# Optimization experiments

Hardware: AMD Instinct MI355X
Metric: run time of the kernel (lower is better)

The kernel has to match this reference:

```python
import jax, jax.numpy as jnp
import numpy as np

START_TAG = 8
STOP_TAG = 9
NEG_INF = -10000.0


def setup_inputs() -> dict:
    key = jax.random.key(0)
    k1, k2, k3 = jax.random.split(key, 3)
    S, B, T = 2048, 4096, 10
    feats = jax.random.normal(k1, (S, B, T), dtype=jnp.float32)
    lengths = jax.random.randint(k2, (B,), 1, S + 1, dtype=jnp.int32)
    transitions = jax.random.normal(k3, (T, T), dtype=jnp.float32)
    # transitions[next, prev]; nothing transitions INTO start, nothing OUT of stop
    transitions = transitions.at[START_TAG, :].set(NEG_INF).at[:, STOP_TAG].set(NEG_INF)
    return {"feats": feats, "transitions": transitions, "lengths": lengths}


def reference(feats, transitions, lengths):
    # Viterbi decode (the module's forward).
    S, B, T = feats.shape
    bidx = jnp.arange(B)
    init = jnp.full((B, T), NEG_INF, feats.dtype).at[:, START_TAG].set(0.0)

    def step(fv, feat):
        # fv: [B, T_prev]; transitions: [T_next, T_prev]
        ntv = fv[:, None, :] + transitions[None, :, :]      # [B, Tn, Tp]
        best = jnp.argmax(ntv, axis=2).astype(jnp.int32)    # [B, Tn]
        fv_new = jnp.max(ntv, axis=2) + feat                # [B, Tn]
        return fv_new, (fv_new, best)

    _, (fv_steps, bptrs) = jax.lax.scan(step, init, feats)
    fv_all = jnp.concatenate([init[None], fv_steps], axis=0)  # [S+1, B, T]

    last_fv = fv_all[lengths, bidx, :]                       # [B, T]
    terminal = last_fv + transitions[STOP_TAG][None, :]
    path_score = jnp.max(terminal, axis=1)                   # [B]
    best_last = jnp.argmax(terminal, axis=1).astype(jnp.int32)

    # Vectorized backtrace over all batches, scanning time in reverse.
    def bt_step(cur, j):
        nxt_j = jnp.minimum(j + 1, S - 1)
        gathered = bptrs[nxt_j, bidx, cur]                   # [B]
        cur_new = jnp.where(j == lengths - 1, best_last,
                  jnp.where(j < lengths - 1, gathered, cur))
        path_j = jnp.where(j < lengths, cur_new, 0)
        return cur_new, path_j

    _, paths_rev = jax.lax.scan(bt_step, best_last, jnp.arange(S - 1, -1, -1))
    best_paths = paths_rev[::-1].T                           # [B, S]
    return path_score, best_paths
```

## Files before the change

### kernel.cpp

```cpp
#include <hip/hip_runtime.h>
#include <stdint.h>
#include <stddef.h>

#define S_LEN 2048
#define B_N   4096
#define T_N   10
#define NCH   128
#define NEG_INF_F (-10000.0f)

template<int CTRL>
__device__ __forceinline__ int dppi(int v) {
    return __builtin_amdgcn_update_dpp(0, v, CTRL, 0xF, 0xF, true);
}

static __device__ __forceinline__ int imin(int a, int b) { return a < b ? a : b; }
static __device__ __forceinline__ int imax(int a, int b) { return a > b ? a : b; }

static __device__ __forceinline__ float vmax3(float a, float b, float c) {
    float d;
    asm("v_max3_f32 %0, %1, %2, %3" : "=v"(d) : "v"(a), "v"(b), "v"(c));
    return d;
}

__global__ void __launch_bounds__(256) viterbi_fwd(const float* __restrict__ feats,
                                                   const float* __restrict__ trans,
                                                   const int* __restrict__ lengths,
                                                   float* __restrict__ ckpt) {
    const float FNINF = __int_as_float(0xff800000);
    const int tid = threadIdx.x;
    const int t   = tid & 15;
    const int b   = blockIdx.x * 16 + (tid >> 4);
    const bool act = (t < T_N);
    const int len = lengths[b];

    int lenW = len;
    lenW = imax(lenW, __shfl_xor(lenW, 16, 64));
    lenW = imax(lenW, __shfl_xor(lenW, 32, 64));
    lenW = __builtin_amdgcn_readfirstlane(lenW);

    int q[16];
    q[0]  = t;
    q[1]  = dppi<0x121>(t);  q[2]  = dppi<0x122>(t);  q[3]  = dppi<0x123>(t);
    q[4]  = dppi<0x124>(t);  q[5]  = dppi<0x125>(t);  q[6]  = dppi<0x126>(t);
    q[7]  = dppi<0x127>(t);  q[8]  = dppi<0x128>(t);  q[9]  = dppi<0x129>(t);
    q[10] = dppi<0x12A>(t);  q[11] = dppi<0x12B>(t);  q[12] = dppi<0x12C>(t);
    q[13] = dppi<0x12D>(t);  q[14] = dppi<0x12E>(t);  q[15] = dppi<0x12F>(t);

    float trr[16];
    #pragma unroll
    for (int r = 0; r < 16; ++r) {
        bool v = act && (q[r] < T_N);
        trr[r] = v ? trans[t * T_N + q[r]] : FNINF;
    }

    const float* fptr = feats + (size_t)b * T_N + imin(t, T_N - 1);
    auto ldfeat = [&](int s) -> float {
        return fptr[(size_t)imin(s, S_LEN - 1) * (B_N * T_N)];
    };

    float fvr;
    {
        float finit = (t == 8) ? 0.0f : NEG_INF_F;
        asm("v_mov_b32 %0, %1\n\ts_nop 1" : "=v"(fvr) : "v"(finit));
    }

    float fA[8], fB[8];
    #pragma unroll
    for (int u = 0; u < 8; ++u) fA[u] = ldfeat(u);

    for (int s0 = 0; s0 < lenW; s0 += 8) {
        #pragma unroll
        for (int u = 0; u < 8; ++u) fB[u] = ldfeat(s0 + 8 + u);

        #pragma unroll
        for (int u = 0; u < 8; ++u) {
            float cd[16];
            cd[0] = fvr + trr[0];
#define DPPADD(N, S) asm("v_add_f32_dpp %0, %1, %2 " S " row_mask:0xf bank_mask:0xf" \
                         : "=v"(cd[N]) : "v"(fvr), "v"(trr[N]))
            DPPADD(1,  "row_ror:1");  DPPADD(2,  "row_ror:2");  DPPADD(3,  "row_ror:3");
            DPPADD(4,  "row_ror:4");  DPPADD(5,  "row_ror:5");  DPPADD(6,  "row_ror:6");
            DPPADD(7,  "row_ror:7");  DPPADD(8,  "row_ror:8");  DPPADD(9,  "row_ror:9");
            DPPADD(10, "row_ror:10"); DPPADD(11, "row_ror:11"); DPPADD(12, "row_ror:12");
            DPPADD(13, "row_ror:13"); DPPADD(14, "row_ror:14"); DPPADD(15, "row_ror:15");
#undef DPPADD
            float x0 = vmax3(cd[0],  cd[1],  cd[2]);
            float x1 = vmax3(cd[3],  cd[4],  cd[5]);
            float x2 = vmax3(cd[6],  cd[7],  cd[8]);
            float x3 = vmax3(cd[9],  cd[10], cd[11]);
            float x4 = vmax3(cd[12], cd[13], cd[14]);
            float y0 = vmax3(x0, x1, x2);
            float y1 = vmax3(x3, x4, cd[15]);
            float mm = fmaxf(y0, y1);
            asm("v_add_f32 %0, %1, %2\n\ts_nop 1" : "=v"(fvr) : "v"(mm), "v"(fA[u]));
        }

        const int snext = s0 + 8;
        if ((snext & 15) == 0) {
            if (act && snext <= len && snext <= S_LEN - 16)
                ckpt[((size_t)(snext >> 4) * B_N + b) * T_N + t] = fvr;
        }
        #pragma unroll
        for (int u = 0; u < 8; ++u) fA[u] = fB[u];
    }
}

__global__ void __launch_bounds__(256) bt_maps(const float* __restrict__ feats,
                                               const float* __restrict__ trans,
                                               const int* __restrict__ lengths,
                                               const float* __restrict__ ckpt,
                                               unsigned* __restrict__ bpd,
                                               unsigned char* __restrict__ bpb,
                                               uint2* __restrict__ gmap,
                                               float* __restrict__ lastfv) {
    const int c = blockIdx.x >> 4;
    const int b = ((blockIdx.x & 15) << 8) + threadIdx.x;
    const int len = lengths[b];
    const int r0 = c * 16;
    const int kl = len - r0;

    if (kl < 0) {
        gmap[(size_t)c * B_N + b] = make_uint2(0x76543210u, 0x98u);
        return;
    }

    float fv[T_N];
    if (c == 0) {
        #pragma unroll
        for (int p = 0; p < T_N; ++p) fv[p] = (p == 8) ? 0.0f : NEG_INF_F;
    } else {
        #pragma unroll
        for (int p = 0; p < T_N; ++p) fv[p] = ckpt[((size_t)c * B_N + b) * T_N + p];
    }

    float* lfp = lastfv + (size_t)b * T_N;
    if (kl == 0) {
        #pragma unroll
        for (int n = 0; n < T_N; ++n) lfp[n] = fv[n];
        gmap[(size_t)c * B_N + b] = make_uint2(0x76543210u, 0x98u);
        return;
    }

    const size_t rstride = (size_t)B_N * T_N;
    const float* fbase = feats + (size_t)b * T_N;

    float buf[T_N];
    {
        const float2* p2 = (const float2*)(fbase + (size_t)r0 * rstride);
        #pragma unroll
        for (int i = 0; i < 5; ++i) { float2 v = p2[i]; buf[2*i] = v.x; buf[2*i+1] = v.y; }
    }

    unsigned Glo = 0x76543210u, Ghi = 0x98u;

    {
        float m[T_N];
        #pragma unroll
        for (int n = 0; n < T_N; ++n) {
            float cd[T_N];
            #pragma unroll
            for (int p = 0; p < T_N; ++p) cd[p] = fv[p] + trans[n * T_N + p];
            float x0 = vmax3(cd[0], cd[1], cd[2]);
            float x1 = vmax3(cd[3], cd[4], cd[5]);
            float x2 = vmax3(cd[6], cd[7], cd[8]);
            m[n] = fmaxf(vmax3(x0, x1, x2), cd[9]);
        }
        #pragma unroll
        for (int n = 0; n < T_N; ++n) fv[n] = m[n] + buf[n];
    }

    #pragma unroll 1
    for (int k = 1; k <= 16; ++k) {
        const int r = r0 + k;
        {
            const float2* p2 = (const float2*)(fbase + (size_t)imin(r, S_LEN - 1) * rstride);
            #pragma unroll
            for (int i = 0; i < 5; ++i) { float2 v = p2[i]; buf[2*i] = v.x; buf[2*i+1] = v.y; }
        }
        if (k == kl) {
            #pragma unroll
            for (int n = 0; n < T_N; ++n) lfp[n] = fv[n];
        }
        unsigned mlo = 0, mhi = 0, nGlo = 0, nGhi = 0;
        unsigned long long G64 = ((unsigned long long)Ghi << 32) | Glo;
        float m[T_N];
        #pragma unroll
        for (int n = 0; n < T_N; ++n) {
            float cd[T_N];
            #pragma unroll
            for (int p = 0; p < T_N; ++p) cd[p] = fv[p] + trans[n * T_N + p];
            float x0 = vmax3(cd[0], cd[1], cd[2]);
            float x1 = vmax3(cd[3], cd[4], cd[5]);
            float x2 = vmax3(cd[6], cd[7], cd[8]);
            float mm = fmaxf(vmax3(x0, x1, x2), cd[9]);
            m[n] = mm;
            int ix = 9;
            #pragma unroll
            for (int p = 8; p >= 0; --p) ix = (cd[p] == mm) ? p : ix;
            unsigned nib = (unsigned)(G64 >> (ix << 2)) & 15u;
            if (n < 8) { mlo |= (unsigned)ix << (4 * n);       nGlo |= nib << (4 * n); }
            else       { mhi |= (unsigned)ix << (4 * (n - 8)); nGhi |= nib << (4 * (n - 8)); }
        }
        if (r < len) {
            bpd[(size_t)r * B_N + b] = mlo;
            bpb[(size_t)r * B_N + b] = (unsigned char)mhi;
            Glo = nGlo; Ghi = nGhi;
        }
        if (k < 16) {
            #pragma unroll
            for (int n = 0; n < T_N; ++n) fv[n] = m[n] + buf[n];
        }
    }

    gmap[(size_t)c * B_N + b] = make_uint2(Glo, Ghi);
}

static __device__ __forceinline__ int bpapply(uint2 w, int cur) {
    unsigned long long w64 = ((unsigned long long)w.y << 32) | (unsigned long long)w.x;
    return (int)((w64 >> (cur * 4)) & 15ULL);
}

__global__ void __launch_bounds__(256) bt_compose(const uint2* __restrict__ gmap,
                                                  const float* __restrict__ lastfv,
                                                  const float* __restrict__ trans,
                                                  unsigned char* __restrict__ entry,
                                                  float* __restrict__ score) {
    const int b = blockIdx.x * 256 + threadIdx.x;

    float term[T_N];
    #pragma unroll
    for (int n = 0; n < T_N; ++n)
        term[n] = lastfv[(size_t)b * T_N + n] + trans[9 * T_N + n];
    float x0 = vmax3(term[0], term[1], term[2]);
    float x1 = vmax3(term[3], term[4], term[5]);
    float x2 = vmax3(term[6], term[7], term[8]);
    float pm = fmaxf(vmax3(x0, x1, x2), term[9]);
    int st = 9;
    #pragma unroll
    for (int n = 8; n >= 0; --n) st = (term[n] == pm) ? n : st;
    score[b] = pm;

    uint2 wA[16], wB[16];
    auto pre = [&](uint2 (&W)[16], int cb) {
        #pragma unroll
        for (int u = 0; u < 16; ++u) W[u] = gmap[(size_t)(cb * 16 + u) * B_N + b];
    };
    auto proc = [&](uint2 (&W)[16], int cb) {
        #pragma unroll
        for (int u = 15; u >= 0; --u) {
            int cc = cb * 16 + u;
            entry[(size_t)cc * B_N + b] = (unsigned char)st;
            st = bpapply(W[u], st);
        }
    };
    pre(wA, 7);
    pre(wB, 6); proc(wA, 7);
    pre(wA, 5); proc(wB, 6);
    pre(wB, 4); proc(wA, 5);
    pre(wA, 3); proc(wB, 4);
    pre(wB, 2); proc(wA, 3);
    pre(wA, 1); proc(wB, 2);
    pre(wB, 0); proc(wA, 1);
    proc(wB, 0);
}

__global__ void __launch_bounds__(256) bt_emit(const unsigned* __restrict__ bpd,
                                               const unsigned char* __restrict__ bpb,
                                               const int* __restrict__ lengths,
                                               const unsigned char* __restrict__ entry,
                                               float* __restrict__ opaths) {
    const int c = blockIdx.x >> 4;
    const int b = ((blockIdx.x & 15) << 8) + threadIdx.x;
    const int len = lengths[b];
    float* op = opaths + (size_t)b * S_LEN + c * 16;

    if (c * 16 >= len) {
        float4 z = make_float4(0.f, 0.f, 0.f, 0.f);
        #pragma unroll
        for (int qq = 0; qq < 4; ++qq) *(float4*)(op + qq * 4) = z;
        return;
    }

    const int r0 = c * 16 + 1;
    unsigned Wd[16], Wb[16];
    #pragma unroll
    for (int u = 0; u < 16; ++u) {
        int r = r0 + u;
        unsigned d = 0x76543210u, h = 0x98u;
        if (r < len) { d = bpd[(size_t)r * B_N + b]; h = bpb[(size_t)r * B_N + b]; }
        Wd[u] = d; Wb[u] = h;
    }

    int cur = entry[(size_t)c * B_N + b];
    float buf[16];
    #pragma unroll
    for (int u = 15; u >= 0; --u) {
        unsigned long long w = ((unsigned long long)Wb[u] << 32) | Wd[u];
        cur = (int)((w >> ((cur * 4) & 63)) & 15ULL);
        buf[u] = (c * 16 + u < len) ? (float)cur : 0.0f;
    }
    #pragma unroll
    for (int qq = 0; qq < 4; ++qq)
        *(float4*)(op + qq * 4) = make_float4(buf[qq*4+0], buf[qq*4+1], buf[qq*4+2], buf[qq*4+3]);
}

extern "C" void kernel_launch(void* const* d_in, const int* in_sizes, int n_in,
                              void* d_out, int out_size, void* d_ws, size_t ws_size,
                              hipStream_t stream) {
    const float* feats   = (const float*)d_in[0];
    const float* trans   = (const float*)d_in[1];
    const int*   lengths = (const int*)d_in[2];
    float* out = (float*)d_out;

    char* w = (char*)d_ws;
    float*         ckpt  = (float*)w;          w += (size_t)NCH * B_N * T_N * 4;
    unsigned*      bpd   = (unsigned*)w;       w += (size_t)(S_LEN + 1) * B_N * 4;
    unsigned char* bpb   = (unsigned char*)w;  w += (size_t)(S_LEN + 1) * B_N;
    uint2*         gmap  = (uint2*)w;          w += (size_t)NCH * B_N * 8;
    unsigned char* entry = (unsigned char*)w;  w += (size_t)NCH * B_N;
    float*         lastfv = (float*)w;

    viterbi_fwd<<<B_N / 16, 256, 0, stream>>>(feats, trans, lengths, ckpt);
    bt_maps   <<<NCH * (B_N / 256), 256, 0, stream>>>(feats, trans, lengths, ckpt, bpd, bpb, gmap, lastfv);
    bt_compose<<<B_N / 256, 256, 0, stream>>>(gmap, lastfv, trans, entry, out);
    bt_emit   <<<NCH * (B_N / 256), 256, 0, stream>>>(bpd, bpb, lengths, entry, out + B_N);
}
```

Baseline: 338.3 us.

## Remap forward Viterbi to four lanes per batch with quad-permute DPP

The forward pass now gives each batch element a group of 4 lanes instead of 16. Tags 0-7 are spread across the quad as two per lane, and tags 8 and 9 are replicated in every lane. Each step uses quad_perm DPP shuffles and per-lane transition registers to compute the max over 10 predecessors for 4 output tags. This removes the 6 idle lanes out of every 16 and cuts the wave count by four (64-thread blocks). In exchange each lane does more arithmetic per step and holds larger feature prefetch buffers (32 floats each), which raises register pressure.

```diff
diff --git a/kernel.cpp b/kernel.cpp
--- a/kernel.cpp
+++ b/kernel.cpp
@@ -12,6 +12,10 @@
 __device__ __forceinline__ int dppi(int v) {
     return __builtin_amdgcn_update_dpp(0, v, CTRL, 0xF, 0xF, true);
 }
+template<int CTRL>
+__device__ __forceinline__ float dppf(float v) {
+    return __int_as_float(dppi<CTRL>(__float_as_int(v)));
+}
 
 static __device__ __forceinline__ int imin(int a, int b) { return a < b ? a : b; }
 static __device__ __forceinline__ int imax(int a, int b) { return a > b ? a : b; }
@@ -22,86 +26,100 @@
     return d;
 }
 
-__global__ void __launch_bounds__(256) viterbi_fwd(const float* __restrict__ feats,
-                                                   const float* __restrict__ trans,
-                                                   const int* __restrict__ lengths,
-                                                   float* __restrict__ ckpt) {
-    const float FNINF = __int_as_float(0xff800000);
+#define QP1 0x39
+#define QP2 0x4E
+#define QP3 0x93
+
+__global__ void __launch_bounds__(64) viterbi_fwd(const float* __restrict__ feats,
+                                                  const float* __restrict__ trans,
+                                                  const int* __restrict__ lengths,
+                                                  float* __restrict__ ckpt) {
     const int tid = threadIdx.x;
-    const int t   = tid & 15;
-    const int b   = blockIdx.x * 16 + (tid >> 4);
-    const bool act = (t < T_N);
+    const int l   = tid & 3;
+    const int b   = blockIdx.x * 16 + (tid >> 2);
     const int len = lengths[b];
 
     int lenW = len;
+    lenW = imax(lenW, __shfl_xor(lenW, 4, 64));
+    lenW = imax(lenW, __shfl_xor(lenW, 8, 64));
     lenW = imax(lenW, __shfl_xor(lenW, 16, 64));
     lenW = imax(lenW, __shfl_xor(lenW, 32, 64));
     lenW = __builtin_amdgcn_readfirstlane(lenW);
 
-    int q[16];
-    q[0]  = t;
-    q[1]  = dppi<0x121>(t);  q[2]  = dppi<0x122>(t);  q[3]  = dppi<0x123>(t);
-    q[4]  = dppi<0x124>(t);  q[5]  = dppi<0x125>(t);  q[6]  = dppi<0x126>(t);
-    q[7]  = dppi<0x127>(t);  q[8]  = dppi<0x128>(t);  q[9]  = dppi<0x129>(t);
-    q[10] = dppi<0x12A>(t);  q[11] = dppi<0x12B>(t);  q[12] = dppi<0x12C>(t);
-    q[13] = dppi<0x12D>(t);  q[14] = dppi<0x12E>(t);  q[15] = dppi<0x12F>(t);
-
-    float trr[16];
-    #pragma unroll
-    for (int r = 0; r < 16; ++r) {
-        bool v = act && (q[r] < T_N);
-        trr[r] = v ? trans[t * T_N + q[r]] : FNINF;
-    }
-
-    const float* fptr = feats + (size_t)b * T_N + imin(t, T_N - 1);
-    auto ldfeat = [&](int s) -> float {
-        return fptr[(size_t)imin(s, S_LEN - 1) * (B_N * T_N)];
-    };
-
-    float fvr;
-    {
-        float finit = (t == 8) ? 0.0f : NEG_INF_F;
-        asm("v_mov_b32 %0, %1\n\ts_nop 1" : "=v"(fvr) : "v"(finit));
-    }
-
-    float fA[8], fB[8];
-    #pragma unroll
-    for (int u = 0; u < 8; ++u) fA[u] = ldfeat(u);
-
-    for (int s0 = 0; s0 < lenW; s0 += 8) {
-        #pragma unroll
-        for (int u = 0; u < 8; ++u) fB[u] = ldfeat(s0 + 8 + u);
-
+    const int q1 = dppi<QP1>(l);
+    const int q2 = dppi<QP2>(l);
+    const int q3 = dppi<QP3>(l);
+
+    int to[4] = { l, 4 + l, 8, 9 };
+    float trAs[4], trA1[4], trA2[4], trA3[4];
+    float trBs[4], trB1[4], trB2[4], trB3[4];
+    float tr8[4], tr9[4];
+    #pragma unroll
+    for (int o = 0; o < 4; ++o) {
+        const float* tr = trans + to[o] * T_N;
+        trAs[o] = tr[l];      trA1[o] = tr[q1];     trA2[o] = tr[q2];     trA3[o] = tr[q3];
+        trBs[o] = tr[4 + l];  trB1[o] = tr[4 + q1]; trB2[o] = tr[4 + q2]; trB3[o] = tr[4 + q3];
+        tr8[o]  = tr[8];      tr9[o]  = tr[9];
+    }
+
+    float a = NEG_INF_F, bv = NEG_INF_F, f8 = 0.0f, f9 = NEG_INF_F;
+
+    const float* fp = feats + (size_t)b * T_N;
+    auto ldf = [&](int s, int k) -> float {
+        return fp[(size_t)imin(s, S_LEN - 1) * (B_N * T_N) + to[k]];
+    };
+
+    float fA[32], fB[32];
+    #pragma unroll
+    for (int u = 0; u < 8; ++u) {
+        #pragma unroll
+        for (int k = 0; k < 4; ++k) fA[u * 4 + k] = ldf(u, k);
+    }
+
+    auto onestep = [&](const float* f) {
+        float rA1 = dppf<QP1>(a),  rA2 = dppf<QP2>(a),  rA3 = dppf<QP3>(a);
+        float rB1 = dppf<QP1>(bv), rB2 = dppf<QP2>(bv), rB3 = dppf<QP3>(bv);
+        float m[4];
+        #pragma unroll
+        for (int o = 0; o < 4; ++o) {
+            float c0 = a   + trAs[o], c1 = rA1 + trA1[o], c2 = rA2 + trA2[o], c3 = rA3 + trA3[o];
+            float c4 = bv  + trBs[o], c5 = rB1 + trB1[o], c6 = rB2 + trB2[o], c7 = rB3 + trB3[o];
+            float c8 = f8 + tr8[o],   c9 = f9 + tr9[o];
+            float x0 = vmax3(c0, c1, c2);
+            float x1 = vmax3(c3, c4, c5);
+            float x2 = vmax3(c6, c7, c8);
+            m[o] = fmaxf(vmax3(x0, x1, x2), c9);
+        }
+        a  = m[0] + f[0];
+        bv = m[1] + f[1];
+        f8 = m[2] + f[2];
+        f9 = m[3] + f[3];
+    };
+    auto step8 = [&](float (&f)[32]) {
+        #pragma unroll
+        for (int u = 0; u < 8; ++u) onestep(&f[u * 4]);
+    };
+    auto loadinto = [&](float (&f)[32], int sbase) {
         #pragma unroll
         for (int u = 0; u < 8; ++u) {
-            float cd[16];
-            cd[0] = fvr + trr[0];
-#define DPPADD(N, S) asm("v_add_f32_dpp %0, %1, %2 " S " row_mask:0xf bank_mask:0xf" \
-                         : "=v"(cd[N]) : "v"(fvr), "v"(trr[N]))
-            DPPADD(1,  "row_ror:1");  DPPADD(2,  "row_ror:2");  DPPADD(3,  "row_ror:3");
-            DPPADD(4,  "row_ror:4");  DPPADD(5,  "row_ror:5");  DPPADD(6,  "row_ror:6");
-            DPPADD(7,  "row_ror:7");  DPPADD(8,  "row_ror:8");  DPPADD(9,  "row_ror:9");
-            DPPADD(10, "row_ror:10"); DPPADD(11, "row_ror:11"); DPPADD(12, "row_ror:12");
-            DPPADD(13, "row_ror:13"); DPPADD(14, "row_ror:14"); DPPADD(15, "row_ror:15");
-#undef DPPADD
-            float x0 = vmax3(cd[0],  cd[1],  cd[2]);
-            float x1 = vmax3(cd[3],  cd[4],  cd[5]);
-            float x2 = vmax3(cd[6],  cd[7],  cd[8]);
-            float x3 = vmax3(cd[9],  cd[10], cd[11]);
-            float x4 = vmax3(cd[12], cd[13], cd[14]);
-            float y0 = vmax3(x0, x1, x2);
-            float y1 = vmax3(x3, x4, cd[15]);
-            float mm = fmaxf(y0, y1);
-            asm("v_add_f32 %0, %1, %2\n\ts_nop 1" : "=v"(fvr) : "v"(mm), "v"(fA[u]));
-        }
-
-        const int snext = s0 + 8;
-        if ((snext & 15) == 0) {
-            if (act && snext <= len && snext <= S_LEN - 16)
-                ckpt[((size_t)(snext >> 4) * B_N + b) * T_N + t] = fvr;
-        }
-        #pragma unroll
-        for (int u = 0; u < 8; ++u) fA[u] = fB[u];
+            #pragma unroll
+            for (int k = 0; k < 4; ++k) f[u * 4 + k] = ldf(sbase + u, k);
+        }
+    };
+    auto ckstore = [&](int snext) {
+        if (snext <= len && snext <= S_LEN - 16) {
+            float* cp = ckpt + ((size_t)(snext >> 4) * B_N + b) * T_N;
+            cp[l] = a; cp[4 + l] = bv;
+            if (l == 0) { cp[8] = f8; cp[9] = f9; }
+        }
+    };
+
+    for (int s0 = 0; s0 < lenW; s0 += 16) {
+        loadinto(fB, s0 + 8);
+        step8(fA);
+        loadinto(fA, s0 + 16);
+        step8(fB);
+        ckstore(s0 + 16);
     }
 }
 
@@ -320,7 +338,7 @@
     unsigned char* entry = (unsigned char*)w;  w += (size_t)NCH * B_N;
     float*         lastfv = (float*)w;
 
-    viterbi_fwd<<<B_N / 16, 256, 0, stream>>>(feats, trans, lengths, ckpt);
+    viterbi_fwd<<<B_N / 16, 64, 0, stream>>>(feats, trans, lengths, ckpt);
     bt_maps   <<<NCH * (B_N / 256), 256, 0, stream>>>(feats, trans, lengths, ckpt, bpd, bpb, gmap, lastfv);
     bt_compose<<<B_N / 256, 256, 0, stream>>>(gmap, lastfv, trans, entry, out);
     bt_emit   <<<NCH * (B_N / 256), 256, 0, stream>>>(bpd, bpb, lengths, entry, out + B_N);
```

Measured after the change: 651.4 us. +92.5%, slower.
